# Performance work log

Measured on AMD Instinct MI355X. Metric: run time of the kernel, lower is better.

The kernel has to match this reference:

```python
import jax, jax.numpy as jnp
import numpy as np

B, S, H, NH = 2, 2048, 1024, 16
DK = H // NH

def setup_inputs() -> dict:
    key = jax.random.key(0)
    ks = jax.random.split(key, 8)
    scale = 0.02
    return {
        "x": jax.random.normal(ks[0], (B, S, H), jnp.float32),
        "mask": jax.random.randint(ks[1], (B, S, S), 0, 2, jnp.int32),
        "alibi": jax.random.normal(ks[2], (1, NH, S, S), jnp.float32),
        "W_q": jax.random.normal(ks[3], (H, H), jnp.float32) * scale,
        "b_q": jnp.zeros((H,), jnp.float32),
        "W_k": jax.random.normal(ks[4], (H, H), jnp.float32) * scale,
        "b_k": jnp.zeros((H,), jnp.float32),
        "W_v": jax.random.normal(ks[5], (H, H), jnp.float32) * scale,
        "b_v": jnp.zeros((H,), jnp.float32),
        "W_o": jax.random.normal(ks[6], (H, H), jnp.float32) * scale,
        "b_o": jnp.zeros((H,), jnp.float32),
    }

def reference(x, mask, alibi, W_q, b_q, W_k, b_k, W_v, b_v, W_o, b_o):
    b, s, h = x.shape
    def split_heads(t):  # [B,S,H] -> [B,NH,S,DK]
        return t.reshape(b, s, NH, DK).transpose(0, 2, 1, 3)
    q = split_heads(x @ W_q + b_q)
    k = split_heads(x @ W_k + b_k)
    v = split_heads(x @ W_v + b_v)
    scores = jnp.einsum("bhqd,bhkd->bhqk", q, k) / jnp.sqrt(jnp.float32(DK))
    scores = scores + alibi
    scores = jnp.where(mask[:, None, :, :] == 0, jnp.float32(-1e9), scores)
    probs = jax.nn.softmax(scores, axis=-1)  # dropout is identity in eval
    ctx = jnp.einsum("bhqk,bhkd->bhqd", probs, v)
    ctx = ctx.transpose(0, 2, 1, 3).reshape(b, s, h)
    return ctx @ W_o + b_o
```

## Files before the change

### kernel.cpp

```cpp
#include <hip/hip_runtime.h>
#include <hip/hip_bf16.h>


#define S_LEN 2048
#define H_DIM 1024
#define N_HEADS 16

typedef __bf16 bf16x8 __attribute__((ext_vector_type(8)));
typedef __bf16 bf16x4 __attribute__((ext_vector_type(4)));
typedef float f32x4 __attribute__((ext_vector_type(4)));
typedef unsigned long long u64;

using gvoid = __attribute__((address_space(1))) void;
using svoid = __attribute__((address_space(3))) void;

static __device__ __forceinline__ f32x4 mfma16(bf16x8 a, bf16x8 b, f32x4 c) {
  return __builtin_amdgcn_mfma_f32_16x16x32_bf16(a, b, c, 0, 0, 0);
}

template <int NCH, int NW>
static __device__ __forceinline__ void stage64(const __bf16* g, int rstride,
                                               __bf16* lds, int wid, int lane) {
#pragma unroll
  for (int i = 0; i < NCH / NW; ++i) {
    int chunk = i * NW + wid;
    int u = chunk * 64 + lane;
    int r = u >> 3, s = u & 7;
    const __bf16* src = g + (size_t)r * rstride + ((s ^ (r & 7)) << 3);
    __builtin_amdgcn_global_load_lds((const gvoid*)src,
                                     (svoid*)(lds + chunk * 512), 16, 0, 0);
  }
}

static __device__ __forceinline__ bf16x8 read_frag(const __bf16* lds, int r,
                                                   int slot) {
  return *(const bf16x8*)(lds + r * 64 + ((slot ^ (r & 7)) << 3));
}

__global__ __launch_bounds__(256) void k_convert_x(const float* __restrict__ x,
                                                   __bf16* __restrict__ xb) {
  size_t idx = ((size_t)blockIdx.x * 256 + threadIdx.x) * 8;
  float4 a = *(const float4*)(x + idx);
  float4 b = *(const float4*)(x + idx + 4);
  bf16x8 o;
  o[0] = (__bf16)a.x; o[1] = (__bf16)a.y; o[2] = (__bf16)a.z; o[3] = (__bf16)a.w;
  o[4] = (__bf16)b.x; o[5] = (__bf16)b.y; o[6] = (__bf16)b.z; o[7] = (__bf16)b.w;
  *(bf16x8*)(xb + idx) = o;
}

__global__ __launch_bounds__(256) void k_transpose_w(
    const float* __restrict__ w0, const float* __restrict__ w1,
    const float* __restrict__ w2, const float* __restrict__ w3,
    __bf16* __restrict__ wt) {
  __shared__ float t[64][65];
  int z = blockIdx.z;
  const float* W = (z == 0) ? w0 : (z == 1) ? w1 : (z == 2) ? w2 : w3;
  __bf16* O = wt + (size_t)z * H_DIM * H_DIM;
  int k0 = blockIdx.x * 64, n0 = blockIdx.y * 64;
  int tid = threadIdx.x;
  {
    int r = tid >> 4, c4 = tid & 15;
#pragma unroll
    for (int i = 0; i < 4; ++i) {
      float4 v = *(const float4*)(W + (size_t)(k0 + r + i * 16) * H_DIM + n0 + c4 * 4);
      t[r + i * 16][c4 * 4 + 0] = v.x;
      t[r + i * 16][c4 * 4 + 1] = v.y;
      t[r + i * 16][c4 * 4 + 2] = v.z;
      t[r + i * 16][c4 * 4 + 3] = v.w;
    }
  }
  __syncthreads();
  {
    int nn = tid >> 2, js = (tid & 3) * 16;
    bf16x8 o0, o1;
#pragma unroll
    for (int j = 0; j < 8; ++j) {
      o0[j] = (__bf16)t[js + j][nn];
      o1[j] = (__bf16)t[js + 8 + j][nn];
    }
    __bf16* dst = O + (size_t)(n0 + nn) * H_DIM + k0 + js;
    *(bf16x8*)dst = o0;
    *(bf16x8*)(dst + 8) = o1;
  }
}

__global__ __launch_bounds__(256) void k_pack_mask(const int* __restrict__ m,
                                                   u64* __restrict__ out) {
  size_t idx = (size_t)blockIdx.x * 256 + threadIdx.x;
  u64 b = __ballot(m[idx] != 0);
  if ((threadIdx.x & 63) == 0) out[idx >> 6] = b;
}

template <int MODE>
__global__ __launch_bounds__(256) void k_gemm(
    const __bf16* __restrict__ A, const __bf16* __restrict__ B0,
    const __bf16* __restrict__ B1, const __bf16* __restrict__ B2,
    const float* __restrict__ bias0, const float* __restrict__ bias1,
    const float* __restrict__ bias2, __bf16* __restrict__ O0,
    __bf16* __restrict__ O1, __bf16* __restrict__ O2, float* __restrict__ Of) {
  __shared__ alignas(16) __bf16 As[128 * 64];
  __shared__ alignas(16) __bf16 Bs[128 * 64];
  int tid = threadIdx.x, wid = tid >> 6, lane = tid & 63;
  int l15 = lane & 15, lg = lane >> 4;
  int nbase = blockIdx.x * 128, mbase = blockIdx.y * 128;
  const __bf16* Bm;
  const float* bias;
  __bf16* Ob;
  float oscale = 1.0f;
  const int zv = (MODE == 0) ? blockIdx.z : 0;
  if (MODE == 0) {
    Bm = (zv == 0) ? B0 : (zv == 1) ? B1 : B2;
    bias = (zv == 0) ? bias0 : (zv == 1) ? bias1 : bias2;
    Ob = (zv == 0) ? O0 : (zv == 1) ? O1 : O2;
    if (zv == 0) oscale = 0.125f;
  } else {
    Bm = B0; bias = bias0; Ob = O0;
  }
  int wrow = wid >> 1, wcol = wid & 1;
  f32x4 zero = {0.f, 0.f, 0.f, 0.f};
  f32x4 acc[4][4];
#pragma unroll
  for (int i = 0; i < 4; ++i)
#pragma unroll
    for (int j = 0; j < 4; ++j) acc[i][j] = zero;

  for (int kb = 0; kb < H_DIM; kb += 64) {
    __syncthreads();
    const __bf16* Abase;
    int arstride;
    if (MODE == 0) {
      Abase = A + (size_t)mbase * H_DIM + kb;
      arstride = H_DIM;
    } else {
      int b = mbase >> 11, q0 = mbase & 2047, head = kb >> 6;
      Abase = A + ((size_t)(b * N_HEADS + head) * S_LEN + q0) * 64;
      arstride = 64;
    }
    stage64<16, 4>(Abase, arstride, As, wid, lane);
    stage64<16, 4>(Bm + (size_t)nbase * H_DIM + kb, H_DIM, Bs, wid, lane);
    __syncthreads();
#pragma unroll
    for (int t = 0; t < 2; ++t) {
      bf16x8 a[4], bfr[4];
#pragma unroll
      for (int i = 0; i < 4; ++i)
        a[i] = read_frag(As, wrow * 64 + i * 16 + l15, t * 4 + lg);
#pragma unroll
      for (int j = 0; j < 4; ++j)
        bfr[j] = read_frag(Bs, wcol * 64 + j * 16 + l15, t * 4 + lg);
#pragma unroll
      for (int i = 0; i < 4; ++i)
#pragma unroll
        for (int j = 0; j < 4; ++j) acc[i][j] = mfma16(a[i], bfr[j], acc[i][j]);
    }
  }
  float bv[4];
#pragma unroll
  for (int j = 0; j < 4; ++j) bv[j] = bias[nbase + wcol * 64 + j * 16 + l15];
#pragma unroll
  for (int i = 0; i < 4; ++i)
#pragma unroll
    for (int j = 0; j < 4; ++j) {
      if (MODE == 0 && zv == 2) {
        int m0 = mbase + wrow * 64 + i * 16 + lg * 4;
        int col = nbase + wcol * 64 + j * 16 + l15;
        bf16x4 u;
#pragma unroll
        for (int r = 0; r < 4; ++r) u[r] = (__bf16)(acc[i][j][r] + bv[j]);
        size_t off =
            (((size_t)(m0 >> 11) * N_HEADS + (col >> 6)) * 64 + (col & 63)) *
                (size_t)S_LEN +
            (m0 & 2047);
        *(bf16x4*)(Ob + off) = u;
      } else {
#pragma unroll
        for (int r = 0; r < 4; ++r) {
          int m = mbase + wrow * 64 + i * 16 + lg * 4 + r;
          int col = nbase + wcol * 64 + j * 16 + l15;
          float v = (acc[i][j][r] + bv[j]) * oscale;
          if (MODE == 0) {
            size_t off =
                (((size_t)(m >> 11) * N_HEADS + (col >> 6)) * S_LEN +
                 (m & 2047)) *
                    64 +
                (col & 63);
            Ob[off] = (__bf16)v;
          } else {
            Of[(size_t)m * H_DIM + col] = v;
          }
        }
      }
    }
}

__global__ __launch_bounds__(512) void k_attn(
    const __bf16* __restrict__ Q, const __bf16* __restrict__ K,
    const __bf16* __restrict__ VT, const float* __restrict__ alibi,
    const u64* __restrict__ maskb, __bf16* __restrict__ ctx) {
  __shared__ alignas(16) __bf16 Ks[2][64 * 64];
  __shared__ alignas(16) __bf16 Vs[64 * 64];
  __shared__ alignas(16) __bf16 Ps[8][16 * 72];
  int tid = threadIdx.x, wid = tid >> 6, lane = tid & 63;
  int l15 = lane & 15, lg = lane >> 4;
  int bh = blockIdx.x;
  int b = bh & 1, h = bh >> 1;
  int qbase = blockIdx.y * 128;
  size_t bho = (size_t)(b * N_HEADS + h);
  const __bf16* Qb = Q + bho * S_LEN * 64;
  const __bf16* Kb = K + bho * S_LEN * 64;
  const __bf16* Vb = VT + bho * 64 * S_LEN;
  const int q = qbase + wid * 16 + l15;

  bf16x8 qa[2];
  {
    const __bf16* qrow = Qb + (size_t)q * 64;
    qa[0] = *(const bf16x8*)(qrow + lg * 8);
    qa[1] = *(const bf16x8*)(qrow + 32 + lg * 8);
  }
  float mrun = -__builtin_inff(), lrun = 0.f;
  f32x4 cacc[4];
  f32x4 zero = {0.f, 0.f, 0.f, 0.f};
#pragma unroll
  for (int c = 0; c < 4; ++c) cacc[c] = zero;

  const float* arow = alibi + ((size_t)h * S_LEN + q) * S_LEN + lg * 4;
  const u64* mrow = maskb + ((size_t)b * S_LEN + q) * (S_LEN / 64);

  stage64<8, 8>(Kb, 64, Ks[0], wid, lane);
  __builtin_amdgcn_sched_barrier(0);
  f32x4 albP[4];
  u64 mskP;
#pragma unroll
  for (int c = 0; c < 4; ++c) albP[c] = *(const f32x4*)(arow + c * 16);
  mskP = mrow[0];
  __builtin_amdgcn_sched_barrier(0);

  for (int t = 0; t < S_LEN / 64; ++t) {
    const int cur = t & 1;
    asm volatile("s_waitcnt vmcnt(5)" ::: "memory");
    __builtin_amdgcn_sched_barrier(0);
    __builtin_amdgcn_s_barrier();
    __builtin_amdgcn_sched_barrier(0);
    stage64<8, 8>(Vb + t * 64, S_LEN, Vs, wid, lane);
    __builtin_amdgcn_sched_barrier(0);
    const int tn = (t + 1 < S_LEN / 64) ? t + 1 : t;
    stage64<8, 8>(Kb + (size_t)tn * 64 * 64, 64, Ks[cur ^ 1], wid, lane);
    __builtin_amdgcn_sched_barrier(0);

    f32x4 sacc[4];
#pragma unroll
    for (int c = 0; c < 4; ++c) sacc[c] = albP[c];
    __builtin_amdgcn_s_setprio(1);
#pragma unroll
    for (int t2 = 0; t2 < 2; ++t2) {
      bf16x8 kf[4];
#pragma unroll
      for (int c = 0; c < 4; ++c)
        kf[c] = read_frag(Ks[cur], c * 16 + l15, t2 * 4 + lg);
#pragma unroll
      for (int c = 0; c < 4; ++c) sacc[c] = mfma16(kf[c], qa[t2], sacc[c]);
    }
    __builtin_amdgcn_s_setprio(0);
    u64 sh = mskP >> (lg * 4);
#pragma unroll
    for (int c = 0; c < 4; ++c)
      albP[c] = *(const f32x4*)(arow + tn * 64 + c * 16);
    mskP = mrow[tn];

    float s[4][4];
    float m16 = -__builtin_inff();
#pragma unroll
    for (int c = 0; c < 4; ++c) {
      unsigned bits = (unsigned)(sh >> (c * 16)) & 0xFu;
#pragma unroll
      for (int r = 0; r < 4; ++r) {
        float v = (bits & (1u << r)) ? sacc[c][r] : -1e9f;
        s[c][r] = v;
        m16 = fmaxf(m16, v);
      }
    }
    m16 = fmaxf(m16, __shfl_xor(m16, 16));
    m16 = fmaxf(m16, __shfl_xor(m16, 32));
    const bool norsc = __all(m16 <= mrun);
    float mn = fmaxf(mrun, m16);
    float scl = __expf(mrun - mn);
    mrun = mn;
    float rs = 0.f;
#pragma unroll
    for (int c = 0; c < 4; ++c)
#pragma unroll
      for (int r = 0; r < 4; ++r) {
        float pe = __expf(s[c][r] - mn);
        s[c][r] = pe;
        rs += pe;
      }
    rs += __shfl_xor(rs, 16);
    rs += __shfl_xor(rs, 32);
    lrun = lrun * scl + rs;
    if (!norsc) {
#pragma unroll
      for (int c = 0; c < 4; ++c) {
        f32x4 v = cacc[c];
        v[0] *= scl; v[1] *= scl; v[2] *= scl; v[3] *= scl;
        cacc[c] = v;
      }
    }
#pragma unroll
    for (int c = 0; c < 4; ++c) {
      bf16x4 u;
#pragma unroll
      for (int r = 0; r < 4; ++r) u[r] = (__bf16)s[c][r];
      *(bf16x4*)(&Ps[wid][l15 * 72 + c * 16 + lg * 4]) = u;
    }
    __builtin_amdgcn_sched_barrier(0);
    asm volatile("s_waitcnt vmcnt(6)" ::: "memory");
    __builtin_amdgcn_sched_barrier(0);
    __builtin_amdgcn_s_barrier();
    __builtin_amdgcn_sched_barrier(0);
    __builtin_amdgcn_s_setprio(1);
#pragma unroll
    for (int t2 = 0; t2 < 2; ++t2) {
      bf16x8 pa = *(const bf16x8*)(&Ps[wid][l15 * 72 + t2 * 32 + lg * 8]);
#pragma unroll
      for (int c = 0; c < 4; ++c) {
        bf16x8 vb = read_frag(Vs, c * 16 + l15, t2 * 4 + lg);
        cacc[c] = mfma16(vb, pa, cacc[c]);
      }
    }
    __builtin_amdgcn_s_setprio(0);
  }
  asm volatile("s_waitcnt vmcnt(0)" ::: "memory");
  float inv = 1.0f / lrun;
#pragma unroll
  for (int c = 0; c < 4; ++c) {
    bf16x4 u;
#pragma unroll
    for (int r = 0; r < 4; ++r) u[r] = (__bf16)(cacc[c][r] * inv);
    *(bf16x4*)(ctx + bho * S_LEN * 64 + (size_t)q * 64 + c * 16 + lg * 4) = u;
  }
}

extern "C" void kernel_launch(void* const* d_in, const int* in_sizes, int n_in,
                              void* d_out, int out_size, void* d_ws,
                              size_t ws_size, hipStream_t stream) {
  const float* x = (const float*)d_in[0];
  const int* mask = (const int*)d_in[1];
  const float* alibi = (const float*)d_in[2];
  const float* Wq = (const float*)d_in[3];
  const float* bq = (const float*)d_in[4];
  const float* Wk = (const float*)d_in[5];
  const float* bk = (const float*)d_in[6];
  const float* Wv = (const float*)d_in[7];
  const float* bv = (const float*)d_in[8];
  const float* Wo = (const float*)d_in[9];
  const float* bo = (const float*)d_in[10];
  float* out = (float*)d_out;
  char* ws = (char*)d_ws;

  const size_t MB = 1u << 20;
  __bf16* xb = (__bf16*)(ws);
  __bf16* wt = (__bf16*)(ws + 8 * MB);
  __bf16* Qb = (__bf16*)(ws + 16 * MB);
  __bf16* Kb = (__bf16*)(ws + 24 * MB);
  __bf16* VTb = (__bf16*)(ws + 32 * MB);
  u64* maskb = (u64*)(ws + 40 * MB);
  __bf16* ctxb = xb;
  __bf16* wtq = wt;
  __bf16* wtk = wt + (1u << 20);
  __bf16* wtv = wt + 2 * (1u << 20);
  __bf16* wto = wt + 3 * (1u << 20);

  k_convert_x<<<dim3(2048), 256, 0, stream>>>(x, xb);
  k_transpose_w<<<dim3(16, 16, 4), 256, 0, stream>>>(Wq, Wk, Wv, Wo, wt);
  k_gemm<0><<<dim3(8, 32, 3), 256, 0, stream>>>(xb, wtq, wtk, wtv, bq, bk, bv,
                                                Qb, Kb, VTb, nullptr);
  k_pack_mask<<<dim3((2 * S_LEN * S_LEN) / 256), 256, 0, stream>>>(mask, maskb);
  k_attn<<<dim3(32, 16), 512, 0, stream>>>(Qb, Kb, VTb, alibi, maskb, ctxb);
  k_gemm<1><<<dim3(8, 32, 1), 256, 0, stream>>>(ctxb, wto, nullptr, nullptr, bo,
                                                nullptr, nullptr, nullptr,
                                                nullptr, nullptr, out);
}
```

Before: 238.4 us.

## Split attention over two key halves and merge partials in a combine kernel

The attention kernel now launches twice as many blocks, each handling half of the key/value sequence, and writes unnormalised fp32 partial outputs plus running max and sum. A new combine kernel rescales and merges the two partials into the bf16 context. This is meant to raise parallelism from 512 blocks so the GPU's compute units are better filled. The cost is an extra launch and extra fp32 traffic for the partial results.

```diff
diff --git a/kernel.cpp b/kernel.cpp
--- a/kernel.cpp
+++ b/kernel.cpp
@@ -196,7 +196,8 @@
 __global__ __launch_bounds__(512) void k_attn(
     const __bf16* __restrict__ Q, const __bf16* __restrict__ K,
     const __bf16* __restrict__ VT, const float* __restrict__ alibi,
-    const u64* __restrict__ maskb, __bf16* __restrict__ ctx) {
+    const u64* __restrict__ maskb, float* __restrict__ Op,
+    float* __restrict__ ml) {
   __shared__ alignas(16) __bf16 Ks[2][64 * 64];
   __shared__ alignas(16) __bf16 Vs[64 * 64];
   __shared__ alignas(16) __bf16 Ps[8][16 * 72];
@@ -205,11 +206,13 @@
   int bh = blockIdx.x;
   int b = bh & 1, h = bh >> 1;
   int qbase = blockIdx.y * 128;
+  const int z = blockIdx.z;
   size_t bho = (size_t)(b * N_HEADS + h);
   const __bf16* Qb = Q + bho * S_LEN * 64;
-  const __bf16* Kb = K + bho * S_LEN * 64;
-  const __bf16* Vb = VT + bho * 64 * S_LEN;
+  const __bf16* Kbz = K + (bho * S_LEN + (size_t)z * 1024) * 64;
+  const __bf16* Vbz = VT + bho * 64 * S_LEN + z * 1024;
   const int q = qbase + wid * 16 + l15;
+  const int NT = 16;
 
   bf16x8 qa[2];
   {
@@ -223,10 +226,12 @@
 #pragma unroll
   for (int c = 0; c < 4; ++c) cacc[c] = zero;
 
-  const float* arow = alibi + ((size_t)h * S_LEN + q) * S_LEN + lg * 4;
-  const u64* mrow = maskb + ((size_t)b * S_LEN + q) * (S_LEN / 64);
-
-  stage64<8, 8>(Kb, 64, Ks[0], wid, lane);
+  const float* arow =
+      alibi + ((size_t)h * S_LEN + q) * S_LEN + z * 1024 + lg * 4;
+  const u64* mrow =
+      maskb + ((size_t)b * S_LEN + q) * (S_LEN / 64) + z * 16;
+
+  stage64<8, 8>(Kbz, 64, Ks[0], wid, lane);
   __builtin_amdgcn_sched_barrier(0);
   f32x4 albP[4];
   u64 mskP;
@@ -235,16 +240,16 @@
   mskP = mrow[0];
   __builtin_amdgcn_sched_barrier(0);
 
-  for (int t = 0; t < S_LEN / 64; ++t) {
+  for (int t = 0; t < NT; ++t) {
     const int cur = t & 1;
     asm volatile("s_waitcnt vmcnt(5)" ::: "memory");
     __builtin_amdgcn_sched_barrier(0);
     __builtin_amdgcn_s_barrier();
     __builtin_amdgcn_sched_barrier(0);
-    stage64<8, 8>(Vb + t * 64, S_LEN, Vs, wid, lane);
-    __builtin_amdgcn_sched_barrier(0);
-    const int tn = (t + 1 < S_LEN / 64) ? t + 1 : t;
-    stage64<8, 8>(Kb + (size_t)tn * 64 * 64, 64, Ks[cur ^ 1], wid, lane);
+    stage64<8, 8>(Vbz + t * 64, S_LEN, Vs, wid, lane);
+    __builtin_amdgcn_sched_barrier(0);
+    const int tn = (t + 1 < NT) ? t + 1 : t;
+    stage64<8, 8>(Kbz + (size_t)tn * 64 * 64, 64, Ks[cur ^ 1], wid, lane);
     __builtin_amdgcn_sched_barrier(0);
 
     f32x4 sacc[4];
@@ -267,7 +272,6 @@
       albP[c] = *(const f32x4*)(arow + tn * 64 + c * 16);
     mskP = mrow[tn];
 
-    float s[4][4];
     float m16 = -__builtin_inff();
 #pragma unroll
     for (int c = 0; c < 4; ++c) {
@@ -275,7 +279,7 @@
 #pragma unroll
       for (int r = 0; r < 4; ++r) {
         float v = (bits & (1u << r)) ? sacc[c][r] : -1e9f;
-        s[c][r] = v;
+        sacc[c][r] = v;
         m16 = fmaxf(m16, v);
       }
     }
@@ -290,8 +294,8 @@
     for (int c = 0; c < 4; ++c)
 #pragma unroll
       for (int r = 0; r < 4; ++r) {
-        float pe = __expf(s[c][r] - mn);
-        s[c][r] = pe;
+        float pe = __expf(sacc[c][r] - mn);
+        sacc[c][r] = pe;
         rs += pe;
       }
     rs += __shfl_xor(rs, 16);
@@ -309,7 +313,7 @@
     for (int c = 0; c < 4; ++c) {
       bf16x4 u;
 #pragma unroll
-      for (int r = 0; r < 4; ++r) u[r] = (__bf16)s[c][r];
+      for (int r = 0; r < 4; ++r) u[r] = (__bf16)sacc[c][r];
       *(bf16x4*)(&Ps[wid][l15 * 72 + c * 16 + lg * 4]) = u;
     }
     __builtin_amdgcn_sched_barrier(0);
@@ -330,14 +334,31 @@
     __builtin_amdgcn_s_setprio(0);
   }
   asm volatile("s_waitcnt vmcnt(0)" ::: "memory");
-  float inv = 1.0f / lrun;
-#pragma unroll
-  for (int c = 0; c < 4; ++c) {
-    bf16x4 u;
-#pragma unroll
-    for (int r = 0; r < 4; ++r) u[r] = (__bf16)(cacc[c][r] * inv);
-    *(bf16x4*)(ctx + bho * S_LEN * 64 + (size_t)q * 64 + c * 16 + lg * 4) = u;
-  }
+  float* op = Op + (((size_t)z * 32 + bho) * S_LEN + q) * 64;
+#pragma unroll
+  for (int c = 0; c < 4; ++c) *(f32x4*)(op + c * 16 + lg * 4) = cacc[c];
+  if (lg == 0) {
+    float2* mlp = (float2*)(ml + (((size_t)z * 32 + bho) * S_LEN + q) * 2);
+    *mlp = make_float2(mrun, lrun);
+  }
+}
+
+__global__ __launch_bounds__(256) void k_combine(const float* __restrict__ Op,
+                                                 const float* __restrict__ ml,
+                                                 __bf16* __restrict__ ctx) {
+  int t = blockIdx.x * 256 + threadIdx.x;
+  int dgrp = t & 15, qq = t >> 4;
+  float2 m0 = *(const float2*)(ml + (size_t)qq * 2);
+  float2 m1 = *(const float2*)(ml + ((size_t)65536 + qq) * 2);
+  float m = fmaxf(m0.x, m1.x);
+  float e0 = __expf(m0.x - m), e1 = __expf(m1.x - m);
+  float inv = 1.f / (m0.y * e0 + m1.y * e1);
+  f32x4 a = *(const f32x4*)(Op + (size_t)qq * 64 + dgrp * 4);
+  f32x4 c = *(const f32x4*)(Op + (size_t)65536 * 64 + (size_t)qq * 64 + dgrp * 4);
+  bf16x4 o;
+#pragma unroll
+  for (int j = 0; j < 4; ++j) o[j] = (__bf16)((a[j] * e0 + c[j] * e1) * inv);
+  *(bf16x4*)(ctx + (size_t)qq * 64 + dgrp * 4) = o;
 }
 
 extern "C" void kernel_launch(void* const* d_in, const int* in_sizes, int n_in,
@@ -364,6 +385,8 @@
   __bf16* Kb = (__bf16*)(ws + 24 * MB);
   __bf16* VTb = (__bf16*)(ws + 32 * MB);
   u64* maskb = (u64*)(ws + 40 * MB);
+  float* Op = (float*)(ws + 48 * MB);
+  float* mlb = (float*)(ws + 112 * MB);
   __bf16* ctxb = xb;
   __bf16* wtq = wt;
   __bf16* wtk = wt + (1u << 20);
@@ -375,7 +398,9 @@
   k_gemm<0><<<dim3(8, 32, 3), 256, 0, stream>>>(xb, wtq, wtk, wtv, bq, bk, bv,
                                                 Qb, Kb, VTb, nullptr);
   k_pack_mask<<<dim3((2 * S_LEN * S_LEN) / 256), 256, 0, stream>>>(mask, maskb);
-  k_attn<<<dim3(32, 16), 512, 0, stream>>>(Qb, Kb, VTb, alibi, maskb, ctxb);
+  k_attn<<<dim3(32, 16, 2), 512, 0, stream>>>(Qb, Kb, VTb, alibi, maskb, Op,
+                                              mlb);
+  k_combine<<<dim3(4096), 256, 0, stream>>>(Op, mlb, ctxb);
   k_gemm<1><<<dim3(8, 32, 1), 256, 0, stream>>>(ctxb, wto, nullptr, nullptr, bo,
                                                 nullptr, nullptr, nullptr,
                                                 nullptr, nullptr, out);
```

Result: no change. 240.5 us (+0.9%).
